# Optimization experiments

Hardware: AMD Instinct MI355X
Metric: run time of the kernel (lower is better)

Reference implementation:

```python
import jax, jax.numpy as jnp
import numpy as np

B, S, D = 2, 2048, 1024
H, KVH = 16, 4
HD = D // H            # 64
REP = H // KVH         # 4
SCALE = HD ** -0.5


def setup_inputs() -> dict:
    key = jax.random.key(0)
    ks = jax.random.split(key, 5)
    x = jax.random.normal(ks[0], (B, S, D), dtype=jnp.float32)
    mask = jnp.ones((B, S), dtype=jnp.int32)
    # torch Linear weights: [out_features, in_features], y = x @ W.T
    Wq = jax.random.normal(ks[1], (D, D), dtype=jnp.float32) * (D ** -0.5)
    Wk = jax.random.normal(ks[2], (KVH * HD, D), dtype=jnp.float32) * (D ** -0.5)
    Wv = jax.random.normal(ks[3], (KVH * HD, D), dtype=jnp.float32) * (D ** -0.5)
    Wo = jax.random.normal(ks[4], (D, D), dtype=jnp.float32) * (D ** -0.5)
    return {"x": x, "mask": mask, "Wq": Wq, "Wk": Wk, "Wv": Wv, "Wo": Wo}


def reference(x, mask, Wq, Wk, Wv, Wo):
    b, s, _ = x.shape
    q = (x @ Wq.T).reshape(b, s, H, HD)          # [B,S,H,HD]
    k = (x @ Wk.T).reshape(b, s, KVH, HD)        # [B,S,KVH,HD]
    v = (x @ Wv.T).reshape(b, s, KVH, HD)
    # repeat_interleave along head dim: each kv head repeated REP times
    k = jnp.repeat(k, REP, axis=2)               # [B,S,H,HD]
    v = jnp.repeat(v, REP, axis=2)
    q = q.transpose(0, 2, 1, 3)                  # [B,H,S,HD]
    k = k.transpose(0, 2, 1, 3)
    v = v.transpose(0, 2, 1, 3)
    scores = jnp.einsum('bhqd,bhkd->bhqk', q, k) * SCALE  # [B,H,S,S]
    m = mask[:, None, None, :]                   # [B,1,1,S]
    scores = jnp.where(m == 0, jnp.float32(-jnp.inf), scores)
    attn = jax.nn.softmax(scores, axis=-1)
    out = jnp.einsum('bhqk,bhkd->bhqd', attn, v) # [B,H,S,HD]
    out = out.transpose(0, 2, 1, 3).reshape(b, s, D)
    return out @ Wo.T
```

## Files before the change

### kernel.cpp

```cpp
#include <hip/hip_runtime.h>
#include <hip/hip_bf16.h>
#include <stdint.h>

#define B_    2
#define S_    2048
#define D_    1024
#define H_    16
#define KVH_  4
#define HD_   64
#define REP_  4
#define BS_   (B_ * S_)
#define KVD_  256
#define QKVS_ 1536
#define NTT_  (S_ / 128)

typedef unsigned short u16;
typedef short s16x4 __attribute__((ext_vector_type(4)));
typedef short s16x8 __attribute__((ext_vector_type(8)));
typedef float f32x4 __attribute__((ext_vector_type(4)));

typedef const __attribute__((address_space(1))) void* gvp;
typedef __attribute__((address_space(3))) void* lvp;

#define MFMA16(a, b, c) __builtin_amdgcn_mfma_f32_16x16x32_bf16((a), (b), (c), 0, 0, 0)

__device__ __forceinline__ u16 f2b(float f) {
  uint32_t u = __float_as_uint(f);
  u += 0x7fffu + ((u >> 16) & 1u);
  return (u16)(u >> 16);
}

__device__ __forceinline__ int swz64(int row, int slot) {
  return slot ^ (row & 7) ^ ((row >> 3) & 7);
}
__device__ __forceinline__ int swz128(int row, int slot) {
  return slot ^ (row & 15);
}

#define N0_ (BS_ * D_ / 4)
#define N1_ (D_ * D_ / 4)
#define N2_ (KVD_ * D_ / 4)
__global__ void cvt5_kernel(const float* __restrict__ s0, const float* __restrict__ s1,
                            const float* __restrict__ s2, const float* __restrict__ s3,
                            const float* __restrict__ s4, u16* __restrict__ dst, int n4tot) {
  for (int i = blockIdx.x * blockDim.x + threadIdx.x; i < n4tot;
       i += gridDim.x * blockDim.x) {
    const float* src;
    int j = i;
    if (j < N0_) src = s0;
    else if ((j -= N0_) < N1_) src = s1;
    else if ((j -= N1_) < N2_) src = s2;
    else if ((j -= N2_) < N2_) src = s3;
    else { j -= N2_; src = s4; }
    const float4 v = reinterpret_cast<const float4*>(src)[j];
    uint2 o;
    o.x = (uint32_t)f2b(v.x) | ((uint32_t)f2b(v.y) << 16);
    o.y = (uint32_t)f2b(v.z) | ((uint32_t)f2b(v.w) << 16);
    reinterpret_cast<uint2*>(dst)[i] = o;
  }
}

template <int OUT_BF16>
__global__ __launch_bounds__(256) void gemm64(const u16* __restrict__ A,
                                              const u16* __restrict__ Bw,
                                              void* __restrict__ Cout,
                                              int M, int N, int K) {
  __shared__ u16 As[64 * 64];
  __shared__ u16 Bs[128 * 64];
  const int tid = threadIdx.x;
  const int lane = tid & 63;
  const int wid = tid >> 6;
  const int l16 = lane & 15;
  const int kq = lane >> 4;
  const int nwg = gridDim.x * gridDim.y;
  const int bid0 = blockIdx.y * gridDim.x + blockIdx.x;
  const int bid = (bid0 & 7) * (nwg >> 3) + (bid0 >> 3);
  const int bm = (bid / gridDim.x) * 64;
  const int bn = (bid % gridDim.x) * 128;
  const int wr = (wid >> 1) * 32;
  const int wc = (wid & 1) * 64;

  int arow[2], acol[2], brow[4], bcol[4], sdst[4];
#pragma unroll
  for (int i = 0; i < 4; ++i) {
    const int e = (i * 256 + tid) * 8;
    const int row = e >> 6;
    const int col = swz64(row, (e >> 3) & 7) * 8;
    sdst[i] = e;
    if (i < 2) { arow[i] = row; acol[i] = col; }
    brow[i] = row;
    bcol[i] = col;
  }
  int aoff[2][2], boff[4][2];
#pragma unroll
  for (int m = 0; m < 2; ++m)
#pragma unroll
    for (int kk = 0; kk < 2; ++kk) {
      const int row = wr + m * 16 + l16;
      aoff[m][kk] = row * 64 + swz64(row, kk * 4 + kq) * 8;
    }
#pragma unroll
  for (int n = 0; n < 4; ++n)
#pragma unroll
    for (int kk = 0; kk < 2; ++kk) {
      const int row = wc + n * 16 + l16;
      boff[n][kk] = row * 64 + swz64(row, kk * 4 + kq) * 8;
    }

  f32x4 acc[2][4] = {};

  for (int kt = 0; kt < K; kt += 64) {
    __syncthreads();
#pragma unroll
    for (int i = 0; i < 2; ++i)
      __builtin_amdgcn_global_load_lds((gvp)(A + (size_t)(bm + arow[i]) * K + kt + acol[i]),
                                       (lvp)(&As[sdst[i]]), 16, 0, 0);
#pragma unroll
    for (int i = 0; i < 4; ++i)
      __builtin_amdgcn_global_load_lds((gvp)(Bw + (size_t)(bn + brow[i]) * K + kt + bcol[i]),
                                       (lvp)(&Bs[sdst[i]]), 16, 0, 0);
    __syncthreads();

#pragma unroll
    for (int kk = 0; kk < 2; ++kk) {
      s16x8 af[2], bfr[4];
#pragma unroll
      for (int m = 0; m < 2; ++m)
        af[m] = *reinterpret_cast<const s16x8*>(&As[aoff[m][kk]]);
#pragma unroll
      for (int n = 0; n < 4; ++n)
        bfr[n] = *reinterpret_cast<const s16x8*>(&Bs[boff[n][kk]]);
#pragma unroll
      for (int m = 0; m < 2; ++m)
#pragma unroll
        for (int n = 0; n < 4; ++n)
          acc[m][n] = MFMA16(af[m], bfr[n], acc[m][n]);
    }
  }

#pragma unroll
  for (int m = 0; m < 2; ++m) {
    const int row0 = bm + wr + m * 16 + kq * 4;
#pragma unroll
    for (int n = 0; n < 4; ++n) {
      const int col = bn + wc + n * 16 + l16;
#pragma unroll
      for (int r = 0; r < 4; ++r) {
        if (OUT_BF16) {
          ((u16*)Cout)[(size_t)(row0 + r) * N + col] = f2b(acc[m][n][r]);
        } else {
          ((float*)Cout)[(size_t)(row0 + r) * N + col] = acc[m][n][r];
        }
      }
    }
  }
}

__global__ __launch_bounds__(256) void vtrans_kernel(const u16* __restrict__ QKV,
                                                     u16* __restrict__ VT) {
  __shared__ u16 T[64][72];
  const int tid = threadIdx.x;
  const int s0 = blockIdx.x * 64;
  const int bg = blockIdx.y;
  const int b = bg >> 2;
  const int g = bg & 3;
  const int r = tid >> 2;
  const int c0 = (tid & 3) * 16;
  const u16* src = QKV + (size_t)(b * S_ + s0 + r) * QKVS_ + D_ + KVD_ + g * HD_ + c0;
  const uint4 a = reinterpret_cast<const uint4*>(src)[0];
  const uint4 bq = reinterpret_cast<const uint4*>(src)[1];
  *reinterpret_cast<uint4*>(&T[r][c0]) = a;
  *reinterpret_cast<uint4*>(&T[r][c0 + 8]) = bq;
  __syncthreads();
  const int d = tid >> 2;
  u16 tmp[16];
#pragma unroll
  for (int j = 0; j < 16; ++j) tmp[j] = T[c0 + j][d];
  u16* dst = VT + ((size_t)bg * 64 + d) * S_ + s0 + c0;
  *reinterpret_cast<uint4*>(dst) = *reinterpret_cast<const uint4*>(&tmp[0]);
  *reinterpret_cast<uint4*>(dst + 8) = *reinterpret_cast<const uint4*>(&tmp[8]);
}

__global__ __launch_bounds__(256, 2) void attn_kernel(const u16* __restrict__ QKV,
                                                      const u16* __restrict__ VT,
                                                      const int* __restrict__ mask,
                                                      u16* __restrict__ O) {
  __shared__ u16 Ks[2][128 * 64];
  __shared__ u16 Vt[2][64 * 128];

  const int tid = threadIdx.x;
  const int lane = tid & 63;
  const int wid = tid >> 6;
  const int l16 = lane & 15;
  const int kq = lane >> 4;
  const int bg = blockIdx.y;
  const int b = bg >> 2;
  const int g = bg & 3;
  const int h = g * REP_ + wid;
  const int q0 = blockIdx.x * 32;
  const u16* kv_base = QKV + (size_t)b * S_ * QKVS_ + D_ + g * HD_;
  const u16* vt_base = VT + (size_t)bg * 64 * S_;
  const int* maskp = mask + b * S_ + lane;
  const float Cs = 0.18033688011112042f;

  int koff[8][2];
#pragma unroll
  for (int n = 0; n < 8; ++n)
#pragma unroll
    for (int c = 0; c < 2; ++c) {
      const int row = n * 16 + l16;
      koff[n][c] = row * 64 + swz64(row, c * 4 + kq) * 8;
    }
  const int hs = kq >> 1;
  const int bo = 4 * (kq & 1);
  int vbase[8];
#pragma unroll
  for (int c = 0; c < 4; ++c) {
    vbase[2 * c] = l16 * 128 + swz128(l16, 4 * c + hs) * 8 + bo;
    vbase[2 * c + 1] = l16 * 128 + swz128(l16, 4 * c + 2 + hs) * 8 + bo;
  }
  int kst_src[4], vst_src[4], st_dst[4];
#pragma unroll
  for (int i = 0; i < 4; ++i) {
    const int e = (i * 256 + tid) * 8;
    st_dst[i] = e;
    const int krow = e >> 6;
    kst_src[i] = krow * QKVS_ + swz64(krow, (e >> 3) & 7) * 8;
    const int vrow = e >> 7;
    vst_src[i] = vrow * S_ + swz128(vrow, (e >> 3) & 15) * 8;
  }

  auto kstage = [&](int buf, int kv0) {
#pragma unroll
    for (int i = 0; i < 4; ++i)
      __builtin_amdgcn_global_load_lds(
          (gvp)(kv_base + (size_t)kv0 * QKVS_ + kst_src[i]),
          (lvp)(&Ks[buf][st_dst[i]]), 16, 0, 0);
  };
  auto vstage = [&](int buf, int kv0) {
#pragma unroll
    for (int i = 0; i < 4; ++i)
      __builtin_amdgcn_global_load_lds(
          (gvp)(vt_base + kv0 + vst_src[i]),
          (lvp)(&Vt[buf][st_dst[i]]), 16, 0, 0);
  };

  s16x8 qf[2][2];
#pragma unroll
  for (int g2 = 0; g2 < 2; ++g2) {
    const u16* qp = QKV + (size_t)(b * S_ + q0 + g2 * 16 + l16) * QKVS_ + h * HD_ + kq * 8;
    qf[g2][0] = *reinterpret_cast<const s16x8*>(qp);
    qf[g2][1] = *reinterpret_cast<const s16x8*>(qp + 32);
  }

  kstage(0, 0);
  vstage(0, 0);
  int mcur0 = maskp[0];
  int mcur1 = maskp[64];

  float m_run[2] = {-1e30f, -1e30f}, l_run[2] = {0.f, 0.f};
  f32x4 acc[2][4] = {};

#define ATTN_TILE(T_, BUF_)                                                       \
  {                                                                               \
    const int t_ = (T_);                                                          \
    __syncthreads();                                                              \
    const bool pfch = (t_ + 1 < NTT_);                                            \
    int mnext0 = 0, mnext1 = 0;                                                   \
    if (pfch) {                                                                   \
      kstage((BUF_) ^ 1, (t_ + 1) * 128);                                         \
      vstage((BUF_) ^ 1, (t_ + 1) * 128);                                         \
      mnext0 = maskp[(t_ + 1) * 128];                                             \
      mnext1 = maskp[(t_ + 1) * 128 + 64];                                        \
    }                                                                             \
    const u16* ks = &Ks[(BUF_)][0];                                               \
    const u16* vt = &Vt[(BUF_)][0];                                               \
    f32x4 sc[2][8];                                                               \
    __builtin_amdgcn_s_setprio(1);                                                \
    _Pragma("unroll") for (int n = 0; n < 8; ++n) {                               \
      const s16x8 kf0 = *reinterpret_cast<const s16x8*>(ks + koff[n][0]);         \
      const s16x8 kf1 = *reinterpret_cast<const s16x8*>(ks + koff[n][1]);         \
      f32x4 s0 = {0.f, 0.f, 0.f, 0.f};                                            \
      f32x4 s1 = {0.f, 0.f, 0.f, 0.f};                                            \
      s0 = MFMA16(kf0, qf[0][0], s0);                                             \
      s1 = MFMA16(kf0, qf[1][0], s1);                                             \
      s0 = MFMA16(kf1, qf[0][1], s0);                                             \
      s1 = MFMA16(kf1, qf[1][1], s1);                                             \
      sc[0][n] = s0;                                                              \
      sc[1][n] = s1;                                                              \
    }                                                                             \
    __builtin_amdgcn_s_setprio(0);                                                \
    const unsigned long long mb0 = __ballot(mcur0 != 0);                          \
    const unsigned long long mb1 = __ballot(mcur1 != 0);                          \
    if ((~mb0) | (~mb1)) {                                                        \
      _Pragma("unroll") for (int n = 0; n < 8; ++n) {                             \
        const unsigned long long mb = (n < 4) ? mb0 : mb1;                        \
        const int sh = (n & 3) * 16 + kq * 4;                                     \
        _Pragma("unroll") for (int r = 0; r < 4; ++r) {                           \
          if (!((mb >> (sh + r)) & 1ull)) {                                       \
            sc[0][n][r] = -3.0e38f;                                               \
            sc[1][n][r] = -3.0e38f;                                               \
          }                                                                       \
        }                                                                         \
      }                                                                           \
    }                                                                             \
    union PK { uint32_t u[16]; s16x8 v[4]; } pk[2];                               \
    _Pragma("unroll") for (int g2 = 0; g2 < 2; ++g2) {                            \
      float tm = -1e30f;                                                          \
      _Pragma("unroll") for (int n = 0; n < 8; ++n)                               \
      _Pragma("unroll") for (int r = 0; r < 4; ++r)                               \
          tm = fmaxf(tm, sc[g2][n][r]);                                           \
      tm = fmaxf(tm, __shfl_xor(tm, 16));                                         \
      tm = fmaxf(tm, __shfl_xor(tm, 32));                                         \
      if (!__all(tm <= m_run[g2] + 44.0f)) {                                      \
        const float mnew = fmaxf(m_run[g2], tm);                                  \
        const float fac = exp2f((m_run[g2] - mnew) * Cs);                         \
        m_run[g2] = mnew;                                                         \
        l_run[g2] *= fac;                                                         \
        _Pragma("unroll") for (int m = 0; m < 4; ++m)                             \
        _Pragma("unroll") for (int r = 0; r < 4; ++r) acc[g2][m][r] *= fac;       \
      }                                                                           \
      float rs = 0.f;                                                             \
      const float mneg = -m_run[g2] * Cs;                                         \
      _Pragma("unroll") for (int n = 0; n < 8; ++n)                               \
      _Pragma("unroll") for (int r = 0; r < 4; ++r) {                             \
        const float p = exp2f(fmaf(sc[g2][n][r], Cs, mneg));                      \
        sc[g2][n][r] = p;                                                         \
        rs += p;                                                                  \
      }                                                                           \
      rs += __shfl_xor(rs, 16);                                                   \
      rs += __shfl_xor(rs, 32);                                                   \
      l_run[g2] += rs;                                                            \
      _Pragma("unroll") for (int n = 0; n < 8; ++n) {                             \
        asm("v_cvt_pk_bf16_f32 %0, %1, %2"                                        \
            : "=v"(pk[g2].u[2 * n]) : "v"(sc[g2][n][0]), "v"(sc[g2][n][1]));      \
        asm("v_cvt_pk_bf16_f32 %0, %1, %2"                                        \
            : "=v"(pk[g2].u[2 * n + 1]) : "v"(sc[g2][n][2]), "v"(sc[g2][n][3])); \
      }                                                                           \
    }                                                                             \
    _Pragma("unroll") for (int m = 0; m < 4; ++m) {                               \
      const u16* vr = vt + m * 2048;                                              \
      s16x8 vfr[4];                                                               \
      _Pragma("unroll") for (int c = 0; c < 4; ++c) {                             \
        union VF { s16x4 h[2]; s16x8 v; } vv;                                     \
        vv.h[0] = *reinterpret_cast<const s16x4*>(vr + vbase[2 * c]);             \
        vv.h[1] = *reinterpret_cast<const s16x4*>(vr + vbase[2 * c + 1]);         \
        vfr[c] = vv.v;                                                            \
      }                                                                           \
      __builtin_amdgcn_s_setprio(1);                                              \
      _Pragma("unroll") for (int c = 0; c < 4; ++c) {                             \
        acc[0][m] = MFMA16(vfr[c], pk[0].v[c], acc[0][m]);                        \
        acc[1][m] = MFMA16(vfr[c], pk[1].v[c], acc[1][m]);                        \
      }                                                                           \
      __builtin_amdgcn_s_setprio(0);                                              \
    }                                                                             \
    mcur0 = mnext0;                                                               \
    mcur1 = mnext1;                                                               \
  }

  for (int t = 0; t < NTT_; t += 2) {
    ATTN_TILE(t, 0)
    ATTN_TILE(t + 1, 1)
  }
#undef ATTN_TILE

#pragma unroll
  for (int g2 = 0; g2 < 2; ++g2) {
    const float rl = 1.0f / l_run[g2];
    u16* op = O + (size_t)(b * S_ + q0 + g2 * 16 + l16) * D_ + h * HD_ + kq * 4;
#pragma unroll
    for (int m = 0; m < 4; ++m) {
      uint2 o;
      o.x = (uint32_t)f2b(acc[g2][m][0] * rl) | ((uint32_t)f2b(acc[g2][m][1] * rl) << 16);
      o.y = (uint32_t)f2b(acc[g2][m][2] * rl) | ((uint32_t)f2b(acc[g2][m][3] * rl) << 16);
      *reinterpret_cast<uint2*>(op + m * 16) = o;
    }
  }
}

extern "C" void kernel_launch(void* const* d_in, const int* in_sizes, int n_in,
                              void* d_out, int out_size, void* d_ws, size_t ws_size,
                              hipStream_t stream) {
  const float* x = (const float*)d_in[0];
  const int* mask = (const int*)d_in[1];
  const float* Wq = (const float*)d_in[2];
  const float* Wk = (const float*)d_in[3];
  const float* Wv = (const float*)d_in[4];
  const float* Wo = (const float*)d_in[5];

  char* w = (char*)d_ws;
  u16* xb = (u16*)w;    w += (size_t)BS_ * D_ * 2;
  u16* Wqkvb = (u16*)w; w += (size_t)QKVS_ * D_ * 2;
  u16* Wob = (u16*)w;   w += (size_t)D_ * D_ * 2;
  u16* QKVw = (u16*)w;  w += (size_t)BS_ * QKVS_ * 2;
  u16* VTw = (u16*)w;   w += (size_t)B_ * KVH_ * HD_ * S_ * 2;
  u16* AOw = (u16*)w;   w += (size_t)BS_ * D_ * 2;

  const int n4tot = (BS_ * D_ + QKVS_ * D_ + D_ * D_) / 4;
  cvt5_kernel<<<dim3(2048), dim3(256), 0, stream>>>(x, Wq, Wk, Wv, Wo, xb, n4tot);

  gemm64<1><<<dim3(QKVS_ / 128, BS_ / 64), dim3(256), 0, stream>>>(xb, Wqkvb, QKVw, BS_, QKVS_, D_);
  vtrans_kernel<<<dim3(S_ / 64, B_ * KVH_), dim3(256), 0, stream>>>(QKVw, VTw);
  attn_kernel<<<dim3(S_ / 32, B_ * KVH_), dim3(256), 0, stream>>>(QKVw, VTw, mask, AOw);
  gemm64<0><<<dim3(D_ / 128, BS_ / 64), dim3(256), 0, stream>>>(AOw, Wob, (float*)d_out, BS_, D_, D_);
}
```

Before: 119.2 us.

## Fuse V transpose into QKV GEMM epilogue and double-buffer GEMM LDS tiles

Removes the separate V-transpose kernel. Output tiles of the QKV GEMM that cover the V columns now write bf16 V directly in transposed [b,g,d,s] layout, packing four consecutive sequence positions per store. The GEMM also gains two-stage LDS buffering, so the next K-tile load is issued before the current tile's MFMAs, with one barrier per iteration instead of two. This trades doubled LDS per block and narrower scattered VT stores for one fewer launch, less global traffic and more load/compute overlap.

Result: faster. 115.6 us (-3.0%).

```diff
diff --git a/kernel.cpp b/kernel.cpp
--- a/kernel.cpp
+++ b/kernel.cpp
@@ -13,6 +13,7 @@
 #define KVD_  256
 #define QKVS_ 1536
 #define NTT_  (S_ / 128)
+#define VSPLIT_ (D_ + KVD_)
 
 typedef unsigned short u16;
 typedef short s16x4 __attribute__((ext_vector_type(4)));
@@ -60,13 +61,14 @@
   }
 }
 
-template <int OUT_BF16>
+template <int OUT_BF16, int WRITE_VT>
 __global__ __launch_bounds__(256) void gemm64(const u16* __restrict__ A,
                                               const u16* __restrict__ Bw,
                                               void* __restrict__ Cout,
+                                              u16* __restrict__ VT,
                                               int M, int N, int K) {
-  __shared__ u16 As[64 * 64];
-  __shared__ u16 Bs[128 * 64];
+  __shared__ u16 As[2][64 * 64];
+  __shared__ u16 Bs[2][128 * 64];
   const int tid = threadIdx.x;
   const int lane = tid & 63;
   const int wid = tid >> 6;
@@ -107,35 +109,61 @@
       boff[n][kk] = row * 64 + swz64(row, kk * 4 + kq) * 8;
     }
 
+  auto stage = [&](int buf, int kt) {
+#pragma unroll
+    for (int i = 0; i < 2; ++i)
+      __builtin_amdgcn_global_load_lds((gvp)(A + (size_t)(bm + arow[i]) * K + kt + acol[i]),
+                                       (lvp)(&As[buf][sdst[i]]), 16, 0, 0);
+#pragma unroll
+    for (int i = 0; i < 4; ++i)
+      __builtin_amdgcn_global_load_lds((gvp)(Bw + (size_t)(bn + brow[i]) * K + kt + bcol[i]),
+                                       (lvp)(&Bs[buf][sdst[i]]), 16, 0, 0);
+  };
+
   f32x4 acc[2][4] = {};
+  stage(0, 0);
+  int cur = 0;
 
   for (int kt = 0; kt < K; kt += 64) {
     __syncthreads();
-#pragma unroll
-    for (int i = 0; i < 2; ++i)
-      __builtin_amdgcn_global_load_lds((gvp)(A + (size_t)(bm + arow[i]) * K + kt + acol[i]),
-                                       (lvp)(&As[sdst[i]]), 16, 0, 0);
-#pragma unroll
-    for (int i = 0; i < 4; ++i)
-      __builtin_amdgcn_global_load_lds((gvp)(Bw + (size_t)(bn + brow[i]) * K + kt + bcol[i]),
-                                       (lvp)(&Bs[sdst[i]]), 16, 0, 0);
-    __syncthreads();
+    if (kt + 64 < K) stage(cur ^ 1, kt + 64);
 
 #pragma unroll
     for (int kk = 0; kk < 2; ++kk) {
       s16x8 af[2], bfr[4];
 #pragma unroll
       for (int m = 0; m < 2; ++m)
-        af[m] = *reinterpret_cast<const s16x8*>(&As[aoff[m][kk]]);
+        af[m] = *reinterpret_cast<const s16x8*>(&As[cur][aoff[m][kk]]);
 #pragma unroll
       for (int n = 0; n < 4; ++n)
-        bfr[n] = *reinterpret_cast<const s16x8*>(&Bs[boff[n][kk]]);
+        bfr[n] = *reinterpret_cast<const s16x8*>(&Bs[cur][boff[n][kk]]);
 #pragma unroll
       for (int m = 0; m < 2; ++m)
 #pragma unroll
         for (int n = 0; n < 4; ++n)
           acc[m][n] = MFMA16(af[m], bfr[n], acc[m][n]);
     }
+    cur ^= 1;
+  }
+
+  if (WRITE_VT && bn >= VSPLIT_) {
+#pragma unroll
+    for (int m = 0; m < 2; ++m) {
+      const int row0 = bm + wr + m * 16 + kq * 4;
+      const int b = row0 >> 11;
+      const int s = row0 & (S_ - 1);
+#pragma unroll
+      for (int n = 0; n < 4; ++n) {
+        const int off = bn - VSPLIT_ + wc + n * 16 + l16;
+        const int g = off >> 6;
+        const int d = off & 63;
+        uint2 o;
+        o.x = (uint32_t)f2b(acc[m][n][0]) | ((uint32_t)f2b(acc[m][n][1]) << 16);
+        o.y = (uint32_t)f2b(acc[m][n][2]) | ((uint32_t)f2b(acc[m][n][3]) << 16);
+        *reinterpret_cast<uint2*>(&VT[((size_t)(b * 4 + g) * 64 + d) * S_ + s]) = o;
+      }
+    }
+    return;
   }
 
 #pragma unroll
@@ -154,31 +182,6 @@
       }
     }
   }
-}
-
-__global__ __launch_bounds__(256) void vtrans_kernel(const u16* __restrict__ QKV,
-                                                     u16* __restrict__ VT) {
-  __shared__ u16 T[64][72];
-  const int tid = threadIdx.x;
-  const int s0 = blockIdx.x * 64;
-  const int bg = blockIdx.y;
-  const int b = bg >> 2;
-  const int g = bg & 3;
-  const int r = tid >> 2;
-  const int c0 = (tid & 3) * 16;
-  const u16* src = QKV + (size_t)(b * S_ + s0 + r) * QKVS_ + D_ + KVD_ + g * HD_ + c0;
-  const uint4 a = reinterpret_cast<const uint4*>(src)[0];
-  const uint4 bq = reinterpret_cast<const uint4*>(src)[1];
-  *reinterpret_cast<uint4*>(&T[r][c0]) = a;
-  *reinterpret_cast<uint4*>(&T[r][c0 + 8]) = bq;
-  __syncthreads();
-  const int d = tid >> 2;
-  u16 tmp[16];
-#pragma unroll
-  for (int j = 0; j < 16; ++j) tmp[j] = T[c0 + j][d];
-  u16* dst = VT + ((size_t)bg * 64 + d) * S_ + s0 + c0;
-  *reinterpret_cast<uint4*>(dst) = *reinterpret_cast<const uint4*>(&tmp[0]);
-  *reinterpret_cast<uint4*>(dst + 8) = *reinterpret_cast<const uint4*>(&tmp[8]);
 }
 
 __global__ __launch_bounds__(256, 2) void attn_kernel(const u16* __restrict__ QKV,
@@ -399,8 +402,9 @@
   const int n4tot = (BS_ * D_ + QKVS_ * D_ + D_ * D_) / 4;
   cvt5_kernel<<<dim3(2048), dim3(256), 0, stream>>>(x, Wq, Wk, Wv, Wo, xb, n4tot);
 
-  gemm64<1><<<dim3(QKVS_ / 128, BS_ / 64), dim3(256), 0, stream>>>(xb, Wqkvb, QKVw, BS_, QKVS_, D_);
-  vtrans_kernel<<<dim3(S_ / 64, B_ * KVH_), dim3(256), 0, stream>>>(QKVw, VTw);
+  gemm64<1, 1><<<dim3(QKVS_ / 128, BS_ / 64), dim3(256), 0, stream>>>(
+      xb, Wqkvb, QKVw, VTw, BS_, QKVS_, D_);
   attn_kernel<<<dim3(S_ / 32, B_ * KVH_), dim3(256), 0, stream>>>(QKVw, VTw, mask, AOw);
-  gemm64<0><<<dim3(D_ / 128, BS_ / 64), dim3(256), 0, stream>>>(AOw, Wob, (float*)d_out, BS_, D_, D_);
-}
+  gemm64<0, 0><<<dim3(D_ / 128, BS_ / 64), dim3(256), 0, stream>>>(
+      AOw, Wob, (float*)d_out, nullptr, BS_, D_, D_);
+}
```
